# Kernel tuning notes

Measured on AMD Instinct MI355X. Metric: run time of the kernel, lower is better.

The kernel has to match this reference:

```python
import math
import jax, jax.numpy as jnp
import numpy as np

TOP_K = 16
LOW_FREQ = 1
MAX_SEL = 32


def setup_inputs() -> dict:
    key = jax.random.key(0)
    x = jax.random.normal(key, (32, 2048, 512), dtype=jnp.float32)
    return {"x": x}


def reference(x):
    # x: (B, T, D)
    B, T, D = x.shape
    dtype = x.dtype

    xf = jnp.fft.rfft(x, axis=1)  # (B, T//2+1, D) complex
    f_full = jnp.fft.rfftfreq(T, d=1.0).astype(dtype)
    if T % 2 == 0:
        xf = xf[:, LOW_FREQ:-1, :]
        f_vec = f_full[LOW_FREQ:-1]
    else:
        xf = xf[:, LOW_FREQ:, :]
        f_vec = f_full[LOW_FREQ:]
    Lf = xf.shape[1]
    K = min(TOP_K, Lf)

    # top-k over frequency axis, per (b, d)
    xf_t = jnp.transpose(xf, (0, 2, 1))  # (B, D, Lf)
    _, idx = jax.lax.top_k(jnp.abs(xf_t), K)  # (B, D, K), sorted descending
    idx = idx[:, :, : min(MAX_SEL, K)]
    Ksel = idx.shape[2]

    x_sel = jnp.take_along_axis(xf_t, idx, axis=2)  # (B, D, Ksel) complex
    f_sel = f_vec[idx]                               # (B, D, Ksel)
    amp = jnp.abs(x_sel).astype(dtype)
    ph = jnp.angle(x_sel).astype(dtype)

    # y[b,t,d] = sum_k amp * cos(2*pi*f*t + phase), t = linspace(0,1,T)
    two_pi_t = (2.0 * math.pi) * jnp.linspace(0.0, 1.0, T, dtype=dtype)  # (T,)

    def step(acc, kin):
        a, f, p = kin  # each (B, D)
        acc = acc + a[..., None] * jnp.cos(f[..., None] * two_pi_t + p[..., None])
        return acc, None

    init = jnp.zeros((B, D, T), dtype)
    ks = (jnp.moveaxis(amp, 2, 0), jnp.moveaxis(f_sel, 2, 0), jnp.moveaxis(ph, 2, 0))
    y_bdt, _ = jax.lax.scan(step, init, ks)
    return jnp.transpose(y_bdt, (0, 2, 1))  # (B, T, D)
```

## Files before the change

kernel.cpp:

```cpp
#include <hip/hip_runtime.h>
#include <math.h>

#ifndef M_PI
#define M_PI 3.14159265358979323846
#endif

constexpr int cB = 32;
constexpr int cT = 2048;
constexpr int cD = 512;
constexpr int cK = 16;
constexpr int TCH = 64;

__device__ __forceinline__ int PZ(int i) { return i + (i >> 4); }

__device__ __forceinline__ float2 twLO(const float2* TW, int e) {
  return TW[PZ(e)];
}
__device__ __forceinline__ float2 twHI(const float2* TW, int e) {
  float2 w = TW[PZ(e - 512)];
  return make_float2(w.y, -w.x);
}
__device__ __forceinline__ float2 twDYN(const float2* TW, int e) {
  float2 w = TW[PZ(e & 511)];
  return (e < 512) ? w : make_float2(w.y, -w.x);
}

__device__ __forceinline__ void bfly(float2& a, float2& b, float wx, float wy) {
  const float tr = a.x - b.x, ti = a.y - b.y;
  a.x += b.x; a.y += b.y;
  b.x = tr * wx - ti * wy;
  b.y = tr * wy + ti * wx;
}

__device__ __forceinline__ void wave_lds_fence() {
  asm volatile("s_waitcnt lgkmcnt(0)" ::: "memory");
  __builtin_amdgcn_sched_barrier(0);
}

template <int S>
__device__ __forceinline__ void pass8(float2* Z, const float2* TW, int B0, int O) {
  float vr[8], vi[8];
#pragma unroll
  for (int m = 0; m < 8; ++m) {
    const float2 z = Z[PZ(B0 + S * m)];
    vr[m] = z.x; vi[m] = z.y;
  }
  constexpr int E1 = 1024 / (4 * S);
  constexpr int E2 = 1024 / (2 * S);
  constexpr int E3 = 1024 / S;
#pragma unroll
  for (int m = 0; m < 4; ++m) {
    const int e = (O + S * m) * E1;
    const float2 w = (m < 2) ? twLO(TW, e) : twHI(TW, e);
    const float ar = vr[m], ai = vi[m], br = vr[m + 4], bi = vi[m + 4];
    vr[m] = ar + br; vi[m] = ai + bi;
    const float tr = ar - br, ti = ai - bi;
    vr[m + 4] = tr * w.x - ti * w.y; vi[m + 4] = tr * w.y + ti * w.x;
  }
#pragma unroll
  for (int q = 0; q < 8; q += 4) {
#pragma unroll
    for (int m2 = 0; m2 < 2; ++m2) {
      const int m = q + m2;
      const int e = (O + S * m2) * E2;
      const float2 w = (m2 == 0) ? twLO(TW, e) : twHI(TW, e);
      const float ar = vr[m], ai = vi[m], br = vr[m + 2], bi = vi[m + 2];
      vr[m] = ar + br; vi[m] = ai + bi;
      const float tr = ar - br, ti = ai - bi;
      vr[m + 2] = tr * w.x - ti * w.y; vi[m + 2] = tr * w.y + ti * w.x;
    }
  }
  {
    const int e = O * E3;
    const float2 w = (S == 1) ? twLO(TW, 0) : twDYN(TW, e);
#pragma unroll
    for (int m = 0; m < 8; m += 2) {
      const float ar = vr[m], ai = vi[m], br = vr[m + 1], bi = vi[m + 1];
      vr[m] = ar + br; vi[m] = ai + bi;
      const float tr = ar - br, ti = ai - bi;
      vr[m + 1] = tr * w.x - ti * w.y; vi[m + 1] = tr * w.y + ti * w.x;
    }
  }
#pragma unroll
  for (int m = 0; m < 8; ++m) Z[PZ(B0 + S * m)] = make_float2(vr[m], vi[m]);
}

__global__ __launch_bounds__(256) void k_fft_topk(const float* __restrict__ x,
                                                  float* __restrict__ amp_out,
                                                  float* __restrict__ kf_out,
                                                  float* __restrict__ ph_out) {
  __shared__ float2 Z[2176];
  __shared__ float2 TW[544];
  __shared__ float  CV[128];
  __shared__ int    CK[128];
  __shared__ int    CC[4];

  const int tid   = threadIdx.x;
  const int lane  = tid & 63;
  const int wave  = tid >> 6;

  const int i_  = blockIdx.x;
  const int c_  = i_ & 7;
  const int j_  = i_ >> 3;
  const int G_  = c_ * 64 + (j_ >> 4);
  const int s_  = j_ & 15;
  const int b     = G_ >> 4;
  const int dpair = ((G_ & 15) << 4) | s_;
  const int d0    = dpair * 2;

  const float2* xp = (const float2*)x + (size_t)b * cT * (cD / 2) + dpair;
  float2 vv[8];
#pragma unroll
  for (int u = 0; u < 8; ++u) {
    vv[u] = xp[(size_t)(tid + 256 * u) * (cD / 2)];
  }

  for (int j = tid; j < 512; j += 256) {
    float s, c;
    __sincosf(-2.0f * (float)M_PI * (float)j * (1.0f / 2048.0f), &s, &c);
    TW[PZ(j)] = make_float2(c, s);
  }

#pragma unroll
  for (int u = 0; u < 2; ++u) {
    const int O = tid + 256 * u;
    float s1, c1, s2, c2;
    __sincosf(-2.0f * (float)M_PI * (float)O * (1.0f / 2048.0f), &s1, &c1);
    __sincosf(-2.0f * (float)M_PI * (float)(2 * O) * (1.0f / 2048.0f), &s2, &c2);
    bfly(vv[u],     vv[u + 4], c1, s1);
    bfly(vv[u + 2], vv[u + 6], s1, -c1);
    bfly(vv[u],     vv[u + 2], c2, s2);
    bfly(vv[u + 4], vv[u + 6], c2, s2);
    Z[PZ(O)]        = vv[u];
    Z[PZ(O + 512)]  = vv[u + 2];
    Z[PZ(O + 1024)] = vv[u + 4];
    Z[PZ(O + 1536)] = vv[u + 6];
  }
  __syncthreads();

  pass8<64>(Z, TW, (tid >> 6) * 512 + (tid & 63), tid & 63);
  wave_lds_fence();
  pass8<8>(Z, TW, (tid >> 3) * 64 + (tid & 7), tid & 7);
  wave_lds_fence();
  pass8<1>(Z, TW, tid * 8, 0);
  __syncthreads();

  const int col  = wave >> 1;
  const int half = wave & 1;
  float v[8];
  int   kk[8];
#pragma unroll
  for (int u = 0; u < 8; ++u) {
    const int k = half * 512 + lane + 64 * u;
    kk[u] = k;
    if (k == 0) { v[u] = -1.0f; continue; }
    const float2 p = Z[PZ((int)(__brev((unsigned)k) >> 21))];
    const float2 q = Z[PZ((int)(__brev((unsigned)(2048 - k)) >> 21))];
    float xr, xi;
    if (col == 0) { xr = p.x + q.x; xi = p.y - q.y; }
    else          { xr = p.y + q.y; xi = q.x - p.x; }
    v[u] = xr * xr + xi * xi;
  }

  {
    float lm = v[0];
#pragma unroll
    for (int j = 1; j < 8; ++j) lm = fmaxf(lm, v[j]);
    float sm = lm;
#pragma unroll
    for (int k2 = 2; k2 <= 64; k2 <<= 1) {
#pragma unroll
      for (int j = k2 >> 1; j > 0; j >>= 1) {
        const float om = __shfl_xor(sm, j);
        const bool wmin = ((lane & k2) == 0) != ((lane & j) == 0);
        const bool oless = (om < sm);
        sm = (oless == wmin) ? om : sm;
      }
    }
    const float thr = __shfl(sm, 16);

    unsigned long long mball[8];
    int cnt = 0;
#pragma unroll
    for (int j = 0; j < 8; ++j) {
      mball[j] = __ballot(v[j] >= thr);
      cnt += __popcll(mball[j]);
    }

    if (cnt <= 32) {
      int pos = 0;
#pragma unroll
      for (int j = 0; j < 8; ++j) {
        const int p = pos + __popcll(mball[j] & ((1ull << lane) - 1ull));
        if (v[j] >= thr) { CV[wave * 32 + p] = v[j]; CK[wave * 32 + p] = kk[j]; }
        pos += __popcll(mball[j]);
      }
      if (lane == 0) CC[wave] = cnt;
    } else {
      float fv[8];
#pragma unroll
      for (int j = 0; j < 8; ++j) fv[j] = v[j];
      for (int it = 0; it < cK + 1; ++it) {
        float bv = fv[0]; int bj = 0;
#pragma unroll
        for (int j = 1; j < 8; ++j) if (fv[j] > bv) { bv = fv[j]; bj = j; }
        int bk = kk[bj];
        for (int off = 32; off > 0; off >>= 1) {
          const float ov = __shfl_down(bv, off);
          const int   ok = __shfl_down(bk, off);
          if (ov > bv) { bv = ov; bk = ok; }
        }
        const int   bkb = __shfl(bk, 0);
        const float bvb = __shfl(bv, 0);
#pragma unroll
        for (int j = 0; j < 8; ++j) if (kk[j] == bkb) fv[j] = -1.0f;
        if (lane == 0) { CV[wave * 32 + it] = bvb; CK[wave * 32 + it] = bkb; }
      }
      if (lane == 0) CC[wave] = cK + 1;
    }
  }
  __syncthreads();

  if ((wave & 1) == 0) {
    const int c0 = CC[wave];
    const int c1 = CC[wave + 1];
    const int n  = c0 + c1;
    float mv = -1.0f;
    int   mk = 5000 + lane;
    if (lane < c0)     { mv = CV[wave * 32 + lane];            mk = CK[wave * 32 + lane]; }
    else if (lane < n) { mv = CV[(wave + 1) * 32 + lane - c0]; mk = CK[(wave + 1) * 32 + lane - c0]; }

#pragma unroll
    for (int k2 = 2; k2 <= 64; k2 <<= 1) {
#pragma unroll
      for (int j = k2 >> 1; j > 0; j >>= 1) {
        const float ov = __shfl_xor(mv, j);
        const int   ok = __shfl_xor(mk, j);
        const bool wmin  = ((lane & k2) == 0) != ((lane & j) == 0);
        const bool oless = (ov < mv) || (ov == mv && ok > mk);
        if (oless == wmin) { mv = ov; mk = ok; }
      }
    }
    const float myv = mv;
    const int   myk = mk;

    const float v15 = __shfl(myv, 15);
    const float v16 = __shfl(myv, 16);
    const int   k15 = __shfl(myk, 15);
    const int   k16 = __shfl(myk, 16);
    bool  do_swap = false;
    double aR = 0.0, pR = 0.0;
    if (v15 - v16 < 1e-3f * v15) {
      const float* colp = x + (size_t)b * cT * cD + (d0 + col);
      double m2[2], XR[2], XI[2];
      for (int bb = 0; bb < 2; ++bb) {
        const int k = bb ? k16 : k15;
        double sr = 0.0, si = 0.0;
        for (int u = 0; u < 32; ++u) {
          const int t = lane + 64 * u;
          const int m = (k * t) & 2047;
          double s, c;
          sincos(-M_PI * (double)m / 1024.0, &s, &c);
          const double xv = (double)colp[(size_t)t * cD];
          sr += xv * c; si += xv * s;
        }
        for (int off = 32; off > 0; off >>= 1) {
          sr += __shfl_down(sr, off);
          si += __shfl_down(si, off);
        }
        sr = __shfl(sr, 0); si = __shfl(si, 0);
        m2[bb] = sr * sr + si * si; XR[bb] = sr; XI[bb] = si;
      }
      if (m2[1] > m2[0]) {
        do_swap = true;
        aR = sqrt(m2[1]);
        pR = atan2(XI[1], XR[1]);
      }
    }

    if (lane < cK) {
      float a, p, kf;
      if (do_swap && lane == 15) {
        a = (float)aR; p = (float)pR; kf = (float)k16;
      } else {
        const int k = myk;
        const float2 zp = Z[PZ((int)(__brev((unsigned)k) >> 21))];
        const float2 zq = Z[PZ((int)(__brev((unsigned)(2048 - k)) >> 21))];
        float xr, xi;
        if (col == 0) { xr = 0.5f * (zp.x + zq.x); xi = 0.5f * (zp.y - zq.y); }
        else          { xr = 0.5f * (zp.y + zq.y); xi = 0.5f * (zq.x - zp.x); }
        a = sqrtf(xr * xr + xi * xi);
        p = atan2f(xi, xr);
        kf = (float)k;
      }
      const size_t cidx = ((size_t)b * cD + (d0 + col)) * cK + lane;
      amp_out[cidx] = a;
      kf_out[cidx]  = kf;
      ph_out[cidx]  = p;
    }
  }
}

__global__ __launch_bounds__(256) void k_recon(const float* __restrict__ amp_in,
                                               const float* __restrict__ kf_in,
                                               const float* __restrict__ ph_in,
                                               float* __restrict__ y) {
  const int tid = threadIdx.x;
  const int d   = blockIdx.y * 256 + tid;
  const int b   = blockIdx.z;
  const int t0  = blockIdx.x * TCH;
  const size_t cidx = ((size_t)b * cD + d) * cK;
  const float Cw = (float)(2.0 * M_PI / (2047.0 * 2048.0));
  const float t0f = (float)t0;

  float amp[cK], kf[cK], ph[cK];
#pragma unroll
  for (int q = 0; q < 4; ++q) {
    const float4 va = ((const float4*)(amp_in + cidx))[q];
    const float4 vk = ((const float4*)(kf_in + cidx))[q];
    const float4 vp = ((const float4*)(ph_in + cidx))[q];
    amp[4*q+0] = va.x; amp[4*q+1] = va.y; amp[4*q+2] = va.z; amp[4*q+3] = va.w;
    kf [4*q+0] = vk.x; kf [4*q+1] = vk.y; kf [4*q+2] = vk.z; kf [4*q+3] = vk.w;
    ph [4*q+0] = vp.x; ph [4*q+1] = vp.y; ph [4*q+2] = vp.z; ph [4*q+3] = vp.w;
  }

  float r[cK], dd[cK], cm[cK];
  float acc0 = 0.0f, acc1 = 0.0f;
#pragma unroll
  for (int j = 0; j < cK; ++j) {
    const float w  = kf[j] * Cw;
    const float w2 = w * w;
    cm[j] = w2 - w2 * w2 * (1.0f / 12.0f);
    const float kt = kf[j] * t0f;
    const float r0 = amp[j] * __cosf(__fmaf_rn(kt, Cw, ph[j]));
    const float r1 = amp[j] * __cosf(__fmaf_rn(kt + kf[j], Cw, ph[j]));
    r[j] = r1; dd[j] = r1 - r0;
    acc0 += r0; acc1 += r1;
  }
  float* yp = y + ((size_t)b * cT + t0) * cD + d;
  yp[0] = acc0;
  yp[cD] = acc1;
  yp += 2 * (size_t)cD;
#pragma unroll 2
  for (int t = 2; t < TCH; ++t) {
    float acc = 0.0f;
#pragma unroll
    for (int j = 0; j < cK; ++j) {
      dd[j] = __fmaf_rn(-cm[j], r[j], dd[j]);
      r[j] += dd[j];
      acc += r[j];
    }
    *yp = acc;
    yp += cD;
  }
}

extern "C" void kernel_launch(void* const* d_in, const int* in_sizes, int n_in,
                              void* d_out, int out_size, void* d_ws, size_t ws_size,
                              hipStream_t stream) {
  const float* x = (const float*)d_in[0];
  float* out = (float*)d_out;

  float* amp = (float*)d_ws;
  float* kf  = amp + (size_t)cB * cD * cK;
  float* ph  = kf + (size_t)cB * cD * cK;

  k_fft_topk<<<cB * cD / 2, 256, 0, stream>>>(x, amp, kf, ph);

  dim3 g3(cT / TCH, cD / 256, cB), b3(256, 1, 1);
  k_recon<<<g3, b3, 0, stream>>>(amp, kf, ph, out);
}
```

Baseline: 334.0 us.

## Process four channels per block with float4 loads and two FFTs per block

The FFT/top-k kernel now handles four adjacent channels per 512-thread block, running two independent complex FFTs (each packing two real columns) in separate LDS buffers. Global loads are widened from float2 to float4, halving the number of strided load instructions and improving per-row coalescing. CV/CK/CC scratch arrays are aliased onto the twiddle buffer to offset the doubled Z footprint. The cost is higher LDS per block and larger blocks, which may reduce occupancy, plus a risk that the aliased scratch overwrites twiddles still in use.

New measurement: 339.4 us. No clear change (+1.6%).

```diff
diff --git a/kernel.cpp b/kernel.cpp
--- a/kernel.cpp
+++ b/kernel.cpp
@@ -85,68 +85,81 @@
   for (int m = 0; m < 8; ++m) Z[PZ(B0 + S * m)] = make_float2(vr[m], vi[m]);
 }
 
-__global__ __launch_bounds__(256) void k_fft_topk(const float* __restrict__ x,
+__global__ __launch_bounds__(512) void k_fft_topk(const float* __restrict__ x,
                                                   float* __restrict__ amp_out,
                                                   float* __restrict__ kf_out,
                                                   float* __restrict__ ph_out) {
-  __shared__ float2 Z[2176];
+  __shared__ float2 Z[2][2176];
   __shared__ float2 TW[544];
-  __shared__ float  CV[128];
-  __shared__ int    CK[128];
-  __shared__ int    CC[4];
-
-  const int tid   = threadIdx.x;
-  const int lane  = tid & 63;
-  const int wave  = tid >> 6;
-
-  const int i_  = blockIdx.x;
-  const int c_  = i_ & 7;
-  const int j_  = i_ >> 3;
-  const int G_  = c_ * 64 + (j_ >> 4);
-  const int s_  = j_ & 15;
+  float* CV = (float*)TW;
+  int*   CK = ((int*)TW) + 256;
+  int*   CC = ((int*)TW) + 512;
+
+  const int tid  = threadIdx.x;
+  const int lane = tid & 63;
+  const int wave = tid >> 6;
+  const int stid = tid & 255;
+  const int sub  = tid >> 8;
+
+  const int i_ = blockIdx.x;
+  const int c_ = i_ & 7;
+  const int j_ = i_ >> 3;
+  const int G_ = c_ * 64 + (j_ >> 3);
+  const int s_ = j_ & 7;
   const int b     = G_ >> 4;
-  const int dpair = ((G_ & 15) << 4) | s_;
-  const int d0    = dpair * 2;
-
-  const float2* xp = (const float2*)x + (size_t)b * cT * (cD / 2) + dpair;
-  float2 vv[8];
-#pragma unroll
-  for (int u = 0; u < 8; ++u) {
-    vv[u] = xp[(size_t)(tid + 256 * u) * (cD / 2)];
-  }
-
-  for (int j = tid; j < 512; j += 256) {
+  const int gpair = ((G_ & 15) << 3) | s_;
+
+  const float4* xq = (const float4*)x + (size_t)b * cT * (cD / 4) + gpair;
+  float4 g[4];
+#pragma unroll
+  for (int u = 0; u < 4; ++u) {
+    g[u] = xq[(size_t)(tid + 512 * u) * (cD / 4)];
+  }
+
+  {
     float s, c;
-    __sincosf(-2.0f * (float)M_PI * (float)j * (1.0f / 2048.0f), &s, &c);
-    TW[PZ(j)] = make_float2(c, s);
-  }
-
-#pragma unroll
-  for (int u = 0; u < 2; ++u) {
-    const int O = tid + 256 * u;
+    __sincosf(-2.0f * (float)M_PI * (float)tid * (1.0f / 2048.0f), &s, &c);
+    TW[PZ(tid)] = make_float2(c, s);
+  }
+
+  {
+    const int O = tid;
     float s1, c1, s2, c2;
     __sincosf(-2.0f * (float)M_PI * (float)O * (1.0f / 2048.0f), &s1, &c1);
     __sincosf(-2.0f * (float)M_PI * (float)(2 * O) * (1.0f / 2048.0f), &s2, &c2);
-    bfly(vv[u],     vv[u + 4], c1, s1);
-    bfly(vv[u + 2], vv[u + 6], s1, -c1);
-    bfly(vv[u],     vv[u + 2], c2, s2);
-    bfly(vv[u + 4], vv[u + 6], c2, s2);
-    Z[PZ(O)]        = vv[u];
-    Z[PZ(O + 512)]  = vv[u + 2];
-    Z[PZ(O + 1024)] = vv[u + 4];
-    Z[PZ(O + 1536)] = vv[u + 6];
+#pragma unroll
+    for (int s = 0; s < 2; ++s) {
+      float2 a0 = s ? make_float2(g[0].z, g[0].w) : make_float2(g[0].x, g[0].y);
+      float2 a1 = s ? make_float2(g[1].z, g[1].w) : make_float2(g[1].x, g[1].y);
+      float2 a2 = s ? make_float2(g[2].z, g[2].w) : make_float2(g[2].x, g[2].y);
+      float2 a3 = s ? make_float2(g[3].z, g[3].w) : make_float2(g[3].x, g[3].y);
+      bfly(a0, a2, c1, s1);
+      bfly(a1, a3, s1, -c1);
+      bfly(a0, a1, c2, s2);
+      bfly(a2, a3, c2, s2);
+      float2* Zs = Z[s];
+      Zs[PZ(O)]        = a0;
+      Zs[PZ(O + 512)]  = a1;
+      Zs[PZ(O + 1024)] = a2;
+      Zs[PZ(O + 1536)] = a3;
+    }
   }
   __syncthreads();
 
-  pass8<64>(Z, TW, (tid >> 6) * 512 + (tid & 63), tid & 63);
-  wave_lds_fence();
-  pass8<8>(Z, TW, (tid >> 3) * 64 + (tid & 7), tid & 7);
-  wave_lds_fence();
-  pass8<1>(Z, TW, tid * 8, 0);
+  {
+    float2* Zs = Z[sub];
+    pass8<64>(Zs, TW, (stid >> 6) * 512 + (stid & 63), stid & 63);
+    wave_lds_fence();
+    pass8<8>(Zs, TW, (stid >> 3) * 64 + (stid & 7), stid & 7);
+    wave_lds_fence();
+    pass8<1>(Zs, TW, stid * 8, 0);
+  }
   __syncthreads();
 
-  const int col  = wave >> 1;
+  const int fft  = wave >> 2;
+  const int col  = (wave >> 1) & 1;
   const int half = wave & 1;
+  const float2* Zf = Z[fft];
   float v[8];
   int   kk[8];
 #pragma unroll
@@ -154,8 +167,8 @@
     const int k = half * 512 + lane + 64 * u;
     kk[u] = k;
     if (k == 0) { v[u] = -1.0f; continue; }
-    const float2 p = Z[PZ((int)(__brev((unsigned)k) >> 21))];
-    const float2 q = Z[PZ((int)(__brev((unsigned)(2048 - k)) >> 21))];
+    const float2 p = Zf[PZ((int)(__brev((unsigned)k) >> 21))];
+    const float2 q = Zf[PZ((int)(__brev((unsigned)(2048 - k)) >> 21))];
     float xr, xi;
     if (col == 0) { xr = p.x + q.x; xi = p.y - q.y; }
     else          { xr = p.y + q.y; xi = q.x - p.x; }
@@ -244,6 +257,8 @@
     const float myv = mv;
     const int   myk = mk;
 
+    const int dcol = (2 * gpair + fft) * 2 + col;
+
     const float v15 = __shfl(myv, 15);
     const float v16 = __shfl(myv, 16);
     const int   k15 = __shfl(myk, 15);
@@ -251,7 +266,7 @@
     bool  do_swap = false;
     double aR = 0.0, pR = 0.0;
     if (v15 - v16 < 1e-3f * v15) {
-      const float* colp = x + (size_t)b * cT * cD + (d0 + col);
+      const float* colp = x + (size_t)b * cT * cD + dcol;
       double m2[2], XR[2], XI[2];
       for (int bb = 0; bb < 2; ++bb) {
         const int k = bb ? k16 : k15;
@@ -284,8 +299,8 @@
         a = (float)aR; p = (float)pR; kf = (float)k16;
       } else {
         const int k = myk;
-        const float2 zp = Z[PZ((int)(__brev((unsigned)k) >> 21))];
-        const float2 zq = Z[PZ((int)(__brev((unsigned)(2048 - k)) >> 21))];
+        const float2 zp = Zf[PZ((int)(__brev((unsigned)k) >> 21))];
+        const float2 zq = Zf[PZ((int)(__brev((unsigned)(2048 - k)) >> 21))];
         float xr, xi;
         if (col == 0) { xr = 0.5f * (zp.x + zq.x); xi = 0.5f * (zp.y - zq.y); }
         else          { xr = 0.5f * (zp.y + zq.y); xi = 0.5f * (zq.x - zp.x); }
@@ -293,7 +308,7 @@
         p = atan2f(xi, xr);
         kf = (float)k;
       }
-      const size_t cidx = ((size_t)b * cD + (d0 + col)) * cK + lane;
+      const size_t cidx = ((size_t)b * cD + dcol) * cK + lane;
       amp_out[cidx] = a;
       kf_out[cidx]  = kf;
       ph_out[cidx]  = p;
@@ -365,7 +380,7 @@
   float* kf  = amp + (size_t)cB * cD * cK;
   float* ph  = kf + (size_t)cB * cD * cK;
 
-  k_fft_topk<<<cB * cD / 2, 256, 0, stream>>>(x, amp, kf, ph);
+  k_fft_topk<<<cB * cD / 4, 512, 0, stream>>>(x, amp, kf, ph);
 
   dim3 g3(cT / TCH, cD / 256, cB), b3(256, 1, 1);
   k_recon<<<g3, b3, 0, stream>>>(amp, kf, ph, out);
```
